# Kernel tuning notes

Measured on AMD Instinct MI355X. Metric: run time of the kernel, lower is better.

The kernel has to match this reference:

```python
import jax, jax.numpy as jnp
import numpy as np
from jax.scipy.linalg import solve_triangular

LS = 0.5414            # frozen GP length scale (_gp_scale.data = 0.5414)
L2 = LS * LS
D = 2
K_OPS = D + 2          # operators: identity, d/dx_i (i=1..d), laplacian
JITTER_KXX = 1e-5
JITTER_AKA = 1e-4
JITTER_YY = 1e-5


def _opiK(xout, xin, l2, d):
    # op_i applied to first arg of RBF kernel -> (bs, k, m, n)
    r = xout[:, :, None, :] - xin[:, None, :, :]            # (bs,m,n,d)
    u = jnp.sum(r * r, axis=-1) / l2                        # (bs,m,n)
    K = jnp.exp(-0.5 * u)
    ri = jnp.moveaxis(r, -1, 1)                             # (bs,d,m,n)
    grad = -(ri / l2) * K[:, None]                          # d/dx_i K
    lap = ((u - d) / l2) * K                                # Lap_x K
    return jnp.concatenate([K[:, None], grad, lap[:, None]], axis=1)


def _opiKopjfull(x, l2, d):
    # op_i on first arg, op_j on second arg -> (bs, k, k, m, m)
    r = x[:, :, None, :] - x[:, None, :, :]
    u = jnp.sum(r * r, axis=-1) / l2
    K = jnp.exp(-0.5 * u)
    ri = jnp.moveaxis(r, -1, 1)                             # (bs,d,m,m)
    gK = (ri / l2) * K[:, None]                             # d/dy_j K
    lapK = ((u - d) / l2) * K                               # Lap K (either arg)
    eye = jnp.eye(d, dtype=x.dtype)[None, :, :, None, None]
    gg = (eye / l2 - ri[:, :, None] * ri[:, None] / (l2 * l2)) * K[:, None, None]  # d/dx_i d/dy_j K
    glap = (ri / (l2 * l2)) * (((2.0 + d - u) * K)[:, None])  # d/dx_i Lap_y K
    laplap = (((u - d) ** 2 - 4.0 * u + 2.0 * d) / (l2 * l2)) * K  # Lap_x Lap_y K
    row0 = jnp.concatenate([K[:, None, None], gK[:, None], lapK[:, None, None]], axis=2)
    rowg = jnp.concatenate([(-gK)[:, :, None], gg, glap[:, :, None]], axis=2)
    rowl = jnp.concatenate([lapK[:, None, None], (-glap)[:, None], laplap[:, None, None]], axis=2)
    return jnp.concatenate([row0, rowg, rowl], axis=1)


def _psd_solve(L, B):
    # (Kxx + jitter I)^{-1} B via Cholesky (stands in for gpytorch inv_matmul/CG)
    y = solve_triangular(L, B, lower=True)
    return solve_triangular(L, y, lower=True, trans=1)


def _forward(xin, meanin, Kin, weight, bias):
    bs, n, c = meanin.shape
    d, k, l2 = D, K_OPS, L2
    xout, m = xin, n
    r = xin[:, :, None, :] - xin[:, None, :, :]
    Kxx = jnp.exp(-0.5 * jnp.sum(r * r, axis=-1) / l2)      # (bs,n,n)
    In = jnp.eye(n, dtype=xin.dtype)
    Lc = jnp.linalg.cholesky(Kxx + JITTER_KXX * In)
    opiKmn = _opiK(xout, xin, l2, d)                        # (bs,k,m,n)
    # posterior mean of op_i applied to the GP
    opimean = (opiKmn.reshape(bs, k * m, n) @ _psd_solve(Lc, meanin)).reshape(bs, k, m, c)
    Amean = jnp.transpose(opimean, (0, 2, 3, 1)).reshape(bs, m, c * k) @ weight.T + bias
    W = weight.reshape(-1, c, k)                            # (cout,c,k)
    W2 = jnp.einsum('oci,ocj->ij', W, W) / W.shape[0]       # (k,k)
    Kxxinvopi = jnp.swapaxes(
        _psd_solve(Lc, jnp.swapaxes(opiKmn.reshape(bs, k * m, n), 1, 2)), 1, 2)  # (bs,km,n)
    interp_weights = jnp.swapaxes(_psd_solve(Lc, Kin), 1, 2)                      # (bs,n,n)
    opi_interp = jnp.transpose((Kxxinvopi @ interp_weights).reshape(bs, k, m, n), (0, 2, 3, 1))  # (bs,m,n,k)
    Ak_interp = (opi_interp @ W2).reshape(bs, m, n * k)
    Im = jnp.eye(m, dtype=xin.dtype)
    AkinA = Ak_interp @ jnp.transpose(opiKmn, (0, 3, 1, 2)).reshape(bs, n * k, m) + JITTER_AKA * Im
    opiKxxxopj = jnp.transpose(
        (Kxxinvopi @ jnp.swapaxes(opiKmn.reshape(bs, k * m, n), 1, 2)).reshape(bs, k, m, k, m),
        (0, 1, 3, 2, 4))                                    # (bs,k,k,m,m)
    ijkyy = _opiKopjfull(xout, l2, d) - opiKxxxopj          # posterior cov of op_i f, op_j f
    AkAyy = jnp.einsum('bijmp,ij->bmp', ijkyy, W2) + JITTER_YY * Im
    full_AKA = AkinA + AkAyy
    return (xout, Amean, full_AKA)


def setup_inputs() -> dict:
    bs, n, cin, cout = 4, 576, 32, 64
    key = jax.random.key(0)
    k1, k2, k3, k4, k5 = jax.random.split(key, 5)
    xin = jax.random.uniform(k1, (bs, n, D), dtype=jnp.float32) * 6.0
    meanin = jax.random.normal(k2, (bs, n, cin), dtype=jnp.float32)
    A = jax.random.normal(k3, (bs, n, n), dtype=jnp.float32) / np.float32(np.sqrt(n))
    Kin = A @ jnp.swapaxes(A, 1, 2) + 0.1 * jnp.eye(n, dtype=jnp.float32)  # PSD covariance
    fan_in = cin * K_OPS
    weight = jax.random.normal(k4, (cout, fan_in), dtype=jnp.float32) / np.float32(np.sqrt(fan_in))
    bias = jax.random.normal(k5, (cout,), dtype=jnp.float32) * 0.01
    return {"xin": xin, "meanin": meanin, "Kin": Kin, "weight": weight, "bias": bias}


def reference(xin, meanin, Kin, weight, bias):
    return _forward(xin, meanin, Kin, weight, bias)
```

## Files before the change

### kernel.cpp

```cpp
#include <hip/hip_runtime.h>
#include <math.h>

#define NPTS 576
#define N2 331776
#define BSZ 4
#define NB 64
#define NT 9

#define INVL2 (1.0f/0.29311396f)

typedef __attribute__((ext_vector_type(8))) short short8v;
typedef __attribute__((ext_vector_type(16))) float f32x16;

__global__ void build_k(const float* __restrict__ xin,
                        float* __restrict__ Kxx, float* __restrict__ opiK,
                        float* __restrict__ out) {
    int idx = blockIdx.x * 256 + threadIdx.x;
    if (idx < 4608) out[idx] = xin[idx];
    int b = idx / N2;
    int rem = idx - b * N2;
    int m = rem / NPTS;
    int nn = rem - m * NPTS;
    const float* xb = xin + (size_t)b * NPTS * 2;
    float xm0 = xb[m*2],  xm1 = xb[m*2+1];
    float xn0 = xb[nn*2], xn1 = xb[nn*2+1];
    float r0 = xm0 - xn0, r1 = xm1 - xn1;
    float u = (r0*r0 + r1*r1) * INVL2;
    float Kv = expf(-0.5f * u);
    Kxx[idx] = Kv + ((m == nn) ? 1e-5f : 0.0f);
    size_t base = (size_t)b * 4 * N2 + rem;
    opiK[base]          = Kv;
    opiK[base + N2]     = -r0 * INVL2 * Kv;
    opiK[base + 2*N2]   = -r1 * INVL2 * Kv;
    opiK[base + 3*N2]   = (u - 2.0f) * INVL2 * Kv;
}

__global__ void w2_k(const float* __restrict__ w, float* __restrict__ W2) {
    __shared__ float red[256];
    int tid = threadIdx.x;
    int pair = tid & 15;
    int slice = tid >> 4;
    int i = pair >> 2, j = pair & 3;
    float s = 0.0f;
    for (int o = slice * 4; o < slice * 4 + 4; ++o)
        for (int c = 0; c < 32; ++c)
            s += w[o*128 + c*4 + i] * w[o*128 + c*4 + j];
    red[tid] = s;
    __syncthreads();
    if (tid < 16) {
        float t = 0.0f;
        #pragma unroll
        for (int k = 0; k < 16; ++k) t += red[pair + 16*k];
        W2[pair] = t * (1.0f/64.0f);
    }
}

__device__ void factor_invert_64(float (*T)[NB+1], float (*V)[NB+1],
                                 float (*tmp)[17], int tid) {
    for (int p = 0; p < 4; ++p) {
        int cp = p * 16;
        if (tid < 64) {
            int r = tid;
            float reg[16];
            #pragma unroll
            for (int q = 0; q < 16; ++q) reg[q] = T[r][cp + q];
            #pragma unroll
            for (int j = 0; j < 16; ++j) {
                int col = cp + j;
                float d2 = __shfl(reg[j], col);
                float d = sqrtf(fmaxf(d2, 1e-12f));
                float lr = (r == col) ? d : reg[j] / d;
                reg[j] = lr;
                #pragma unroll
                for (int q = j + 1; q < 16; ++q) {
                    float lc = __shfl(lr, cp + q);
                    if (r >= cp + q) reg[q] -= lr * lc;
                }
            }
            #pragma unroll
            for (int q = 0; q < 16; ++q) T[r][cp + q] = reg[q];
        }
        __syncthreads();
        int tr = 48 - cp;
        if (tr > 0) {
            for (int idx = tid; idx < tr * tr; idx += 256) {
                int r = cp + 16 + idx / tr;
                int c = cp + 16 + idx % tr;
                if (c <= r) {
                    float s = 0.0f;
                    #pragma unroll
                    for (int k = 0; k < 16; ++k) s += T[r][cp+k] * T[c][cp+k];
                    T[r][c] -= s;
                }
            }
        }
        __syncthreads();
    }
    if (tid < 64) {
        int I = tid >> 4, c = tid & 15, base = I * 16;
        float tcol[16];
        #pragma unroll
        for (int i = 0; i < 16; ++i) tcol[i] = T[base + i][base + c];
        float v[16];
        #pragma unroll
        for (int i = 0; i < 16; ++i) {
            float s = (i == c) ? 1.0f : 0.0f;
            #pragma unroll
            for (int k = 0; k < 16; ++k) {
                if (k < i) {
                    float tik = __shfl(tcol[i], base + k);
                    s -= tik * v[k];
                }
            }
            float tii = __shfl(tcol[i], base + i);
            v[i] = s / tii;
        }
        #pragma unroll
        for (int i = 0; i < 16; ++i) V[base + i][base + c] = v[i];
    }
    __syncthreads();
    const int PI[6] = {1,2,3,2,3,3};
    const int PJ[6] = {0,1,2,0,1,0};
    int rr16 = tid >> 4, cc16 = tid & 15;
    for (int p = 0; p < 6; ++p) {
        int I = PI[p], J = PJ[p];
        float s = 0.0f;
        for (int K = J; K < I; ++K)
            #pragma unroll
            for (int t = 0; t < 16; ++t)
                s += T[I*16+rr16][K*16+t] * V[K*16+t][J*16+cc16];
        tmp[rr16][cc16] = s;
        __syncthreads();
        float s2 = 0.0f;
        for (int t = 0; t <= rr16; ++t) s2 += V[I*16+rr16][I*16+t] * tmp[t][cc16];
        __syncthreads();
        V[I*16+rr16][J*16+cc16] = -s2;
        __syncthreads();
    }
}

__global__ void chol_diag0(const float* __restrict__ A, float* __restrict__ LinvKK,
                           float* __restrict__ VTKK) {
    int b = blockIdx.x;
    const float* Ab = A + (size_t)b * N2;
    __shared__ float T[NB][NB+1];
    __shared__ float V[NB][NB+1];
    __shared__ float tmp[16][17];
    int tid = threadIdx.x;
    for (int idx = tid; idx < NB*NB; idx += 256) {
        int r = idx >> 6, c = idx & 63;
        T[r][c] = Ab[(size_t)r * NPTS + c];
        V[r][c] = 0.0f;
    }
    __syncthreads();
    factor_invert_64(T, V, tmp, tid);
    float* Vg  = LinvKK + (size_t)b * NT * NB * NB;
    float* VTg = VTKK  + (size_t)b * NT * NB * NB;
    for (int idx = tid; idx < NB*NB; idx += 256) {
        Vg[idx]  = V[idx >> 6][idx & 63];
        VTg[idx] = V[idx & 63][idx >> 6];
    }
}

__global__ __launch_bounds__(256)
void chol_step(float* __restrict__ A, float* __restrict__ LT,
               float* __restrict__ LinvKK, float* __restrict__ VTKK, int kb) {
    int b = blockIdx.y;
    int p = blockIdx.x;
    int ir = 0;
    while (p >= ir + 1) { p -= ir + 1; ir++; }
    int ib = kb + 1 + ir, jb = kb + 1 + p;
    float* Ab = A + (size_t)b * N2;
    float* LTb = LT + (size_t)b * N2;
    __shared__ float Ai[NB][NB+1];
    __shared__ float Aj[NB][NB+1];
    __shared__ float Vs[NB][NB+1];
    __shared__ float tmp[16][17];
    int tid = threadIdx.x;
    int tx = tid & 15, ty = tid >> 4;
    const float* Vg = LinvKK + ((size_t)b * NT + kb) * NB * NB;
    bool diag = (ib == jb);
    for (int idx = tid; idx < NB*NB; idx += 256) {
        int r = idx >> 6, c = idx & 63;
        Ai[r][c] = Ab[(size_t)(ib*NB + r) * NPTS + kb*NB + c];
        Aj[r][c] = diag ? 0.0f : Ab[(size_t)(jb*NB + r) * NPTS + kb*NB + c];
        Vs[r][c] = Vg[idx];
    }
    float U[4][4];
    #pragma unroll
    for (int i = 0; i < 4; ++i)
        #pragma unroll
        for (int j = 0; j < 4; ++j)
            U[i][j] = Ab[(size_t)(ib*NB + ty*4+i) * NPTS + jb*NB + tx*4+j];
    __syncthreads();
    float Li[4][4] = {}, Lj[4][4] = {};
    for (int k = 0; k < NB; ++k) {
        float a[4], v[4];
        #pragma unroll
        for (int i = 0; i < 4; ++i) a[i] = Ai[ty*4+i][k];
        #pragma unroll
        for (int j = 0; j < 4; ++j) v[j] = Vs[tx*4+j][k];
        #pragma unroll
        for (int i = 0; i < 4; ++i)
            #pragma unroll
            for (int j = 0; j < 4; ++j) Li[i][j] += a[i] * v[j];
        if (!diag) {
            float aj[4];
            #pragma unroll
            for (int i = 0; i < 4; ++i) aj[i] = Aj[ty*4+i][k];
            #pragma unroll
            for (int i = 0; i < 4; ++i)
                #pragma unroll
                for (int j = 0; j < 4; ++j) Lj[i][j] += aj[i] * v[j];
        }
    }
    __syncthreads();
    #pragma unroll
    for (int i = 0; i < 4; ++i)
        #pragma unroll
        for (int j = 0; j < 4; ++j) {
            Ai[ty*4+i][tx*4+j] = Li[i][j];
            Aj[ty*4+i][tx*4+j] = diag ? Li[i][j] : Lj[i][j];
        }
    if (diag) {
        #pragma unroll
        for (int i = 0; i < 4; ++i)
            #pragma unroll
            for (int j = 0; j < 4; ++j)
                LTb[(size_t)(kb*NB + tx*4+j) * NPTS + ib*NB + ty*4+i] = Li[i][j];
    }
    __syncthreads();
    float s[4][4] = {};
    for (int k = 0; k < NB; ++k) {
        float a[4], v[4];
        #pragma unroll
        for (int i = 0; i < 4; ++i) a[i] = Ai[ty*4+i][k];
        #pragma unroll
        for (int j = 0; j < 4; ++j) v[j] = Aj[tx*4+j][k];
        #pragma unroll
        for (int i = 0; i < 4; ++i)
            #pragma unroll
            for (int j = 0; j < 4; ++j) s[i][j] += a[i] * v[j];
    }
    #pragma unroll
    for (int i = 0; i < 4; ++i)
        #pragma unroll
        for (int j = 0; j < 4; ++j) U[i][j] -= s[i][j];
    if (blockIdx.x != 0) {
        #pragma unroll
        for (int i = 0; i < 4; ++i)
            #pragma unroll
            for (int j = 0; j < 4; ++j)
                Ab[(size_t)(ib*NB + ty*4+i) * NPTS + jb*NB + tx*4+j] = U[i][j];
        return;
    }
    __syncthreads();
    #pragma unroll
    for (int i = 0; i < 4; ++i)
        #pragma unroll
        for (int j = 0; j < 4; ++j) Ai[ty*4+i][tx*4+j] = U[i][j];
    for (int idx = tid; idx < NB*NB; idx += 256) Aj[idx >> 6][idx & 63] = 0.0f;
    __syncthreads();
    factor_invert_64(Ai, Aj, tmp, tid);
    float* Vo  = LinvKK + ((size_t)b * NT + (kb + 1)) * NB * NB;
    float* VTo = VTKK  + ((size_t)b * NT + (kb + 1)) * NB * NB;
    for (int idx = tid; idx < NB*NB; idx += 256) {
        Vo[idx]  = Aj[idx >> 6][idx & 63];
        VTo[idx] = Aj[idx & 63][idx >> 6];
    }
}

__global__ __launch_bounds__(256)
void trinv_blk(const float* __restrict__ LT, const float* __restrict__ LinvKK,
               const float* __restrict__ VTKK, float* __restrict__ Linv) {
    int sp = blockIdx.x, jb = blockIdx.y, b = blockIdx.z;
    const float* LTb = LT + (size_t)b * N2;
    float* Xg = Linv + (size_t)b * N2;
    const float* Vg  = LinvKK + (size_t)b * NT * NB * NB;
    const float* VTg = VTKK  + (size_t)b * NT * NB * NB;
    int c0 = jb * NB + sp * 16;

    __shared__ float LsT[64][72];
    __shared__ float Xc[576][17];
    __shared__ float Ss[64][17];

    int tid = threadIdx.x;
    int tx = tid & 15, ty = tid >> 4;
    int st = tid >> 2, sc = (tid & 3) * 16;

    {
        const float* Vjj = Vg + (size_t)jb * NB * NB;
        int r = tid >> 2, c4 = (tid & 3) * 4;
        float4 v = *(const float4*)(Vjj + r * NB + sp * 16 + c4);
        Xc[r][c4+0] = v.x; Xc[r][c4+1] = v.y; Xc[r][c4+2] = v.z; Xc[r][c4+3] = v.w;
        *(float4*)(Xg + (size_t)(jb * NB + r) * NPTS + c0 + c4) = v;
    }
    __syncthreads();

    for (int ib = jb + 1; ib < NT; ++ib) {
        float acc[4] = {};
        for (int kb = jb; kb < ib; ++kb) {
            {
                const float* src = LTb + (size_t)(kb * NB + st) * NPTS + ib * NB + sc;
                #pragma unroll
                for (int q = 0; q < 4; ++q)
                    *(float4*)&LsT[st][sc + q*4] = *(const float4*)(src + q*4);
            }
            __syncthreads();
            int xbase = (kb - jb) * 64;
            #pragma unroll 8
            for (int t = 0; t < 64; ++t) {
                float a4[4]; *(float4*)a4 = *(const float4*)&LsT[t][ty*4];
                float xv = Xc[xbase + t][tx];
                #pragma unroll
                for (int i = 0; i < 4; ++i) acc[i] += a4[i] * xv;
            }
            __syncthreads();
        }
        #pragma unroll
        for (int i = 0; i < 4; ++i) Ss[ty*4+i][tx] = acc[i];
        {
            const float* VTi = VTg + (size_t)ib * NB * NB;
            const float* src = VTi + st * NB + sc;
            #pragma unroll
            for (int q = 0; q < 4; ++q)
                *(float4*)&LsT[st][sc + q*4] = *(const float4*)(src + q*4);
        }
        __syncthreads();
        float acc2[4] = {};
        #pragma unroll 8
        for (int t = 0; t < 64; ++t) {
            float a4[4]; *(float4*)a4 = *(const float4*)&LsT[t][ty*4];
            float sv = Ss[t][tx];
            #pragma unroll
            for (int i = 0; i < 4; ++i) acc2[i] += a4[i] * sv;
        }
        int obase = (ib - jb) * 64;
        #pragma unroll
        for (int i = 0; i < 4; ++i) {
            float v = -acc2[i];
            Xc[obase + ty*4 + i][tx] = v;
            Xg[(size_t)(ib * NB + ty*4 + i) * NPTS + c0 + tx] = v;
        }
        __syncthreads();
    }
}

__device__ inline void split3(float v, unsigned short& h0, unsigned short& h1,
                              unsigned short& h2) {
    unsigned u0 = __float_as_uint(v) & 0xffff0000u;
    float f0 = __uint_as_float(u0);
    float r1 = v - f0;
    unsigned u1 = __float_as_uint(r1) & 0xffff0000u;
    float f1 = __uint_as_float(u1);
    float r2 = r1 - f1;
    h0 = (unsigned short)(u0 >> 16);
    h1 = (unsigned short)(u1 >> 16);
    h2 = (unsigned short)((__float_as_uint(r2) + 0x8000u) >> 16);
}

__device__ inline void pack_store(unsigned short* dst, const unsigned short* v) {
    uint4 w;
    w.x = (unsigned)v[0] | ((unsigned)v[1] << 16);
    w.y = (unsigned)v[2] | ((unsigned)v[3] << 16);
    w.z = (unsigned)v[4] | ((unsigned)v[5] << 16);
    w.w = (unsigned)v[6] | ((unsigned)v[7] << 16);
    *(uint4*)dst = w;
}

template<int EPIB>
__global__ __launch_bounds__(256, 2)
void mm_p2_mfma(const float* __restrict__ Aall, const float* __restrict__ Ball,
                float* __restrict__ Call, long sA, long sB, long sC)
{
    int id = blockIdx.x;
    int x8 = id & 7, qq = id >> 3;
    int nx = qq % 9;
    int band = x8 + 8 * (qq / 9);
    if (band >= 18 * BSZ) return;
    int t  = band % 18;
    int b  = band / 18;
    int pp = t / 9, my = t % 9;
    const float* A0 = Aall + (size_t)b * sA + (size_t)(pp * 2) * N2;
    const float* A1 = A0 + N2;
    const float* B  = Ball + (size_t)b * sB;
    float* C0 = Call + (size_t)b * sC + (size_t)(pp * 2) * N2;
    float* C1 = C0 + N2;
    int n0 = nx * 64, m0 = my * 64;

    __shared__ __align__(16) unsigned short As[12][2][64][8];
    __shared__ __align__(16) unsigned short Bs[6][2][64][8];

    int tid  = threadIdx.x;
    int lane = tid & 63;
    int wid  = tid >> 6;
    int wr = wid >> 1, wc = wid & 1;

    f32x16 acc0, acc1;
    #pragma unroll
    for (int i = 0; i < 16; ++i) { acc0[i] = 0.0f; acc1[i] = 0.0f; }

    int ap   = tid >> 7;
    int aq   = tid & 127;
    int ar   = aq >> 1;
    int asub = aq & 1;
    const float* Apl = ap ? A1 : A0;
    int areg = ar >> 5;
    int aln  = ar & 31;

    int bc   = tid & 63;
    int bkg  = tid >> 6;
    int bsub = bkg >> 1;
    int bln  = (bc & 31) + 32 * (bkg & 1);
    int bwc  = bc >> 5;

    float av[16];
    float bv[8];

    auto loadA = [&](int k0) {
        const float* p = Apl + (size_t)(m0 + ar) * 576 + k0 + asub * 16;
        float4 t0 = *(const float4*)(p);
        float4 t1 = *(const float4*)(p + 4);
        float4 t2 = *(const float4*)(p + 8);
        float4 t3 = *(const float4*)(p + 12);
        av[0]=t0.x;  av[1]=t0.y;  av[2]=t0.z;  av[3]=t0.w;
        av[4]=t1.x;  av[5]=t1.y;  av[6]=t1.z;  av[7]=t1.w;
        av[8]=t2.x;  av[9]=t2.y;  av[10]=t2.z; av[11]=t2.w;
        av[12]=t3.x; av[13]=t3.y; av[14]=t3.z; av[15]=t3.w;
    };
    auto loadB = [&](int k0) {
        const float* p = B + (size_t)(k0 + bkg * 8) * 576 + n0 + bc;
        #pragma unroll
        for (int j = 0; j < 8; ++j) {
            float v = p[(size_t)j * 576];
            if (EPIB) { if (k0 + bkg * 8 + j == n0 + bc) v -= 1.0f; }
            bv[j] = v;
        }
    };
    auto storeA = [&]() {
        unsigned short s0[16], s1[16], s2[16];
        #pragma unroll
        for (int j = 0; j < 16; ++j) split3(av[j], s0[j], s1[j], s2[j]);
        #pragma unroll
        for (int h = 0; h < 2; ++h) {
            int ln = aln + 32 * h;
            pack_store(&As[(ap*3 + 0)*2 + areg][asub][ln][0], &s0[8*h]);
            pack_store(&As[(ap*3 + 1)*2 + areg][asub][ln][0], &s1[8*h]);
            pack_store(&As[(ap*3 + 2)*2 + areg][asub][ln][0], &s2[8*h]);
        }
    };
    auto storeB = [&]() {
        unsigned short s0[8], s1[8], s2[8];
        #pragma unroll
        for (int j = 0; j < 8; ++j) split3(bv[j], s0[j], s1[j], s2[j]);
        pack_store(&Bs[0*2 + bwc][bsub][bln][0], s0);
        pack_store(&Bs[1*2 + bwc][bsub][bln][0], s1);
        pack_store(&Bs[2*2 + bwc][bsub][bln][0], s2);
    };

    const short8v* Af = (const short8v*)As;
    const short8v* Bf = (const short8v*)Bs;

    loadA(0); loadB(0);
    for (int k0 = 0; k0 < 576; k0 += 32) {
        storeA(); storeB();
        __syncthreads();
        if (k0 + 32 < 576) { loadA(k0 + 32); loadB(k0 + 32); }
        #pragma unroll
        for (int sub = 0; sub < 2; ++sub) {
            short8v b0 = Bf[((0*2 + wc)*2 + sub)*64 + lane];
            short8v b1 = Bf[((1*2 + wc)*2 + sub)*64 + lane];
            short8v b2 = Bf[((2*2 + wc)*2 + sub)*64 + lane];
            short8v a0 = Af[((0*3 + 0)*2 + wr)*128 + sub*64 + lane];
            short8v a1 = Af[((0*3 + 1)*2 + wr)*128 + sub*64 + lane];
            short8v a2 = Af[((0*3 + 2)*2 + wr)*128 + sub*64 + lane];
            acc0 = __builtin_amdgcn_mfma_f32_32x32x16_bf16(a0, b0, acc0, 0, 0, 0);
            acc0 = __builtin_amdgcn_mfma_f32_32x32x16_bf16(a0, b1, acc0, 0, 0, 0);
            acc0 = __builtin_amdgcn_mfma_f32_32x32x16_bf16(a1, b0, acc0, 0, 0, 0);
            acc0 = __builtin_amdgcn_mfma_f32_32x32x16_bf16(a1, b1, acc0, 0, 0, 0);
            acc0 = __builtin_amdgcn_mfma_f32_32x32x16_bf16(a0, b2, acc0, 0, 0, 0);
            acc0 = __builtin_amdgcn_mfma_f32_32x32x16_bf16(a2, b0, acc0, 0, 0, 0);
            a0 = Af[((1*3 + 0)*2 + wr)*128 + sub*64 + lane];
            a1 = Af[((1*3 + 1)*2 + wr)*128 + sub*64 + lane];
            a2 = Af[((1*3 + 2)*2 + wr)*128 + sub*64 + lane];
            acc1 = __builtin_amdgcn_mfma_f32_32x32x16_bf16(a0, b0, acc1, 0, 0, 0);
            acc1 = __builtin_amdgcn_mfma_f32_32x32x16_bf16(a0, b1, acc1, 0, 0, 0);
            acc1 = __builtin_amdgcn_mfma_f32_32x32x16_bf16(a1, b0, acc1, 0, 0, 0);
            acc1 = __builtin_amdgcn_mfma_f32_32x32x16_bf16(a1, b1, acc1, 0, 0, 0);
            acc1 = __builtin_amdgcn_mfma_f32_32x32x16_bf16(a0, b2, acc1, 0, 0, 0);
            acc1 = __builtin_amdgcn_mfma_f32_32x32x16_bf16(a2, b0, acc1, 0, 0, 0);
        }
        __syncthreads();
    }

    int colg = n0 + 32*wc + (lane & 31);
    int rowb = m0 + 32*wr + 4*(lane >> 5);
    #pragma unroll
    for (int reg = 0; reg < 16; ++reg) {
        int row = rowb + (reg & 3) + 8*(reg >> 2);
        C0[(size_t)row * 576 + colg] = acc0[reg];
        C1[(size_t)row * 576 + colg] = acc1[reg];
    }
}

__global__ __launch_bounds__(256, 2)
void mm_abt_mfma(const float* __restrict__ Aall, const float* __restrict__ Ball,
                 float* __restrict__ Call, long sA, long sB, long sC, long sSplit)
{
    int p = blockIdx.x;
    int ir = 0;
    while (p >= ir + 1) { p -= ir + 1; ir++; }
    int my = ir, nx = p;
    int zz = blockIdx.z;
    int sp = zz & 3, b = zz >> 2;
    const float* A = Aall + (size_t)b * sA + (size_t)sp * N2;
    const float* B = Ball + (size_t)b * sB + (size_t)sp * N2;
    float* Cp = Call + (size_t)b * sC + (size_t)sp * sSplit;
    int m0 = my * 64, n0 = nx * 64;

    __shared__ __align__(16) unsigned short Fr[12][2][64][8];

    int tid  = threadIdx.x;
    int lane = tid & 63;
    int wid  = tid >> 6;
    int wr = wid >> 1, wc = wid & 1;

    f32x16 acc;
    #pragma unroll
    for (int i = 0; i < 16; ++i) acc[i] = 0.0f;

    int sel  = tid >> 7;
    int q2   = tid & 127;
    int r    = q2 >> 1;
    int ssub = q2 & 1;
    const float* Src = sel ? B : A;
    int base0 = sel ? n0 : m0;
    int rreg = r >> 5;
    int rln  = r & 31;

    float av[16];

    auto loadF = [&](int k0) {
        const float* pp = Src + (size_t)(base0 + r) * 576 + k0 + ssub * 16;
        float4 t0 = *(const float4*)(pp);
        float4 t1 = *(const float4*)(pp + 4);
        float4 t2 = *(const float4*)(pp + 8);
        float4 t3 = *(const float4*)(pp + 12);
        av[0]=t0.x;  av[1]=t0.y;  av[2]=t0.z;  av[3]=t0.w;
        av[4]=t1.x;  av[5]=t1.y;  av[6]=t1.z;  av[7]=t1.w;
        av[8]=t2.x;  av[9]=t2.y;  av[10]=t2.z; av[11]=t2.w;
        av[12]=t3.x; av[13]=t3.y; av[14]=t3.z; av[15]=t3.w;
    };
    auto storeF = [&]() {
        unsigned short s0[16], s1[16], s2[16];
        #pragma unroll
        for (int j = 0; j < 16; ++j) split3(av[j], s0[j], s1[j], s2[j]);
        #pragma unroll
        for (int h = 0; h < 2; ++h) {
            int ln = rln + 32 * h;
            pack_store(&Fr[sel*6 + 0*2 + rreg][ssub][ln][0], &s0[8*h]);
            pack_store(&Fr[sel*6 + 1*2 + rreg][ssub][ln][0], &s1[8*h]);
            pack_store(&Fr[sel*6 + 2*2 + rreg][ssub][ln][0], &s2[8*h]);
        }
    };

    const short8v* Ff = (const short8v*)Fr;

    loadF(0);
    for (int k0 = 0; k0 < 576; k0 += 32) {
        storeF();
        __syncthreads();
        if (k0 + 32 < 576) loadF(k0 + 32);
        #pragma unroll
        for (int sub = 0; sub < 2; ++sub) {
            short8v a0 = Ff[((0*2 + wr)*2 + sub)*64 + lane];
            short8v a1 = Ff[((1*2 + wr)*2 + sub)*64 + lane];
            short8v a2 = Ff[((2*2 + wr)*2 + sub)*64 + lane];
            short8v b0 = Ff[((6 + 0*2 + wc)*2 + sub)*64 + lane];
            short8v b1 = Ff[((6 + 1*2 + wc)*2 + sub)*64 + lane];
            short8v b2 = Ff[((6 + 2*2 + wc)*2 + sub)*64 + lane];
            acc = __builtin_amdgcn_mfma_f32_32x32x16_bf16(a0, b0, acc, 0, 0, 0);
            acc = __builtin_amdgcn_mfma_f32_32x32x16_bf16(a0, b1, acc, 0, 0, 0);
            acc = __builtin_amdgcn_mfma_f32_32x32x16_bf16(a1, b0, acc, 0, 0, 0);
            acc = __builtin_amdgcn_mfma_f32_32x32x16_bf16(a1, b1, acc, 0, 0, 0);
            acc = __builtin_amdgcn_mfma_f32_32x32x16_bf16(a0, b2, acc, 0, 0, 0);
            acc = __builtin_amdgcn_mfma_f32_32x32x16_bf16(a2, b0, acc, 0, 0, 0);
        }
        __syncthreads();
    }

    int colg = n0 + 32*wc + (lane & 31);
    int rowb = m0 + 32*wr + 4*(lane >> 5);
    #pragma unroll
    for (int reg = 0; reg < 16; ++reg) {
        int row = rowb + (reg & 3) + 8*(reg >> 2);
        Cp[(size_t)row * 576 + colg] = acc[reg];
    }
}

__global__ __launch_bounds__(256, 2)
void mm_ata_mfma(const float* __restrict__ Lg, float* __restrict__ C,
                 long sA, long sC)
{
    int p = blockIdx.x;
    int ir = 0;
    while (p >= ir + 1) { p -= ir + 1; ir++; }
    int my = ir, nx = p;
    int b = blockIdx.z;
    const float* A = Lg + (size_t)b * sA;
    float* Cb = C + (size_t)b * sC;
    int m0 = my * 64, n0 = nx * 64;
    int kBeg = m0;

    __shared__ __align__(16) unsigned short Fr[12][2][64][8];

    int tid  = threadIdx.x;
    int lane = tid & 63;
    int wid  = tid >> 6;
    int wr = wid >> 1, wc = wid & 1;

    f32x16 acc;
    #pragma unroll
    for (int i = 0; i < 16; ++i) acc[i] = 0.0f;

    int sel  = tid >> 7;
    int q2   = tid & 127;
    int col  = q2 & 63;
    int ssub = q2 >> 6;
    int c0base = sel ? n0 : m0;
    int rreg = col >> 5;
    int rln  = col & 31;

    float av[16];

    auto loadF = [&](int k0) {
        const float* pp = A + (size_t)(k0 + ssub * 16) * 576 + c0base + col;
        #pragma unroll
        for (int j = 0; j < 16; ++j) av[j] = pp[(size_t)j * 576];
    };
    auto storeF = [&]() {
        unsigned short s0[16], s1[16], s2[16];
        #pragma unroll
        for (int j = 0; j < 16; ++j) split3(av[j], s0[j], s1[j], s2[j]);
        #pragma unroll
        for (int h = 0; h < 2; ++h) {
            int ln = rln + 32 * h;
            pack_store(&Fr[sel*6 + 0*2 + rreg][ssub][ln][0], &s0[8*h]);
            pack_store(&Fr[sel*6 + 1*2 + rreg][ssub][ln][0], &s1[8*h]);
            pack_store(&Fr[sel*6 + 2*2 + rreg][ssub][ln][0], &s2[8*h]);
        }
    };

    const short8v* Ff = (const short8v*)Fr;

    loadF(kBeg);
    for (int k0 = kBeg; k0 < 576; k0 += 32) {
        storeF();
        __syncthreads();
        if (k0 + 32 < 576) loadF(k0 + 32);
        #pragma unroll
        for (int sub = 0; sub < 2; ++sub) {
            short8v a0 = Ff[((0*2 + wr)*2 + sub)*64 + lane];
            short8v a1 = Ff[((1*2 + wr)*2 + sub)*64 + lane];
            short8v a2 = Ff[((2*2 + wr)*2 + sub)*64 + lane];
            short8v b0 = Ff[((6 + 0*2 + wc)*2 + sub)*64 + lane];
            short8v b1 = Ff[((6 + 1*2 + wc)*2 + sub)*64 + lane];
            short8v b2 = Ff[((6 + 2*2 + wc)*2 + sub)*64 + lane];
            acc = __builtin_amdgcn_mfma_f32_32x32x16_bf16(a0, b0, acc, 0, 0, 0);
            acc = __builtin_amdgcn_mfma_f32_32x32x16_bf16(a0, b1, acc, 0, 0, 0);
            acc = __builtin_amdgcn_mfma_f32_32x32x16_bf16(a1, b0, acc, 0, 0, 0);
            acc = __builtin_amdgcn_mfma_f32_32x32x16_bf16(a1, b1, acc, 0, 0, 0);
            acc = __builtin_amdgcn_mfma_f32_32x32x16_bf16(a0, b2, acc, 0, 0, 0);
            acc = __builtin_amdgcn_mfma_f32_32x32x16_bf16(a2, b0, acc, 0, 0, 0);
        }
        __syncthreads();
    }

    int colg = n0 + 32*wc + (lane & 31);
    int rowb = m0 + 32*wr + 4*(lane >> 5);
    #pragma unroll
    for (int reg = 0; reg < 16; ++reg) {
        int row = rowb + (reg & 3) + 8*(reg >> 2);
        float v = acc[reg];
        Cb[(size_t)row * 576 + colg] = v;
        Cb[(size_t)colg * 576 + row] = v;
    }
}

__global__ __launch_bounds__(256, 2)
void mm_ab_mfma(const float* __restrict__ Aall, const float* __restrict__ Ball,
                float* __restrict__ Call, long sA, long sB, long sC)
{
    int nx = blockIdx.x % 9, my = blockIdx.x / 9;
    int b = blockIdx.z;
    const float* A = Aall + (size_t)b * sA;
    const float* B = Ball + (size_t)b * sB;
    float* Cb = Call + (size_t)b * sC;
    int m0 = my * 64, n0 = nx * 64;

    __shared__ __align__(16) unsigned short Fr[12][2][64][8];

    int tid  = threadIdx.x;
    int lane = tid & 63;
    int wid  = tid >> 6;
    int wr = wid >> 1, wc = wid & 1;

    f32x16 acc;
    #pragma unroll
    for (int i = 0; i < 16; ++i) acc[i] = 0.0f;

    int sel  = tid >> 7;
    int q2   = tid & 127;
    int ar   = q2 >> 1;
    int asub = q2 & 1;
    int areg = ar >> 5, aln = ar & 31;
    int bcol = q2 & 63;
    int bssub = q2 >> 6;
    int breg = bcol >> 5, brln = bcol & 31;

    float av[16];

    auto loadF = [&](int k0) {
        if (sel == 0) {
            const float* pp = A + (size_t)(m0 + ar) * 576 + k0 + asub * 16;
            float4 t0 = *(const float4*)(pp);
            float4 t1 = *(const float4*)(pp + 4);
            float4 t2 = *(const float4*)(pp + 8);
            float4 t3 = *(const float4*)(pp + 12);
            av[0]=t0.x;  av[1]=t0.y;  av[2]=t0.z;  av[3]=t0.w;
            av[4]=t1.x;  av[5]=t1.y;  av[6]=t1.z;  av[7]=t1.w;
            av[8]=t2.x;  av[9]=t2.y;  av[10]=t2.z; av[11]=t2.w;
            av[12]=t3.x; av[13]=t3.y; av[14]=t3.z; av[15]=t3.w;
        } else {
            const float* pp = B + (size_t)(k0 + bssub * 16) * 576 + n0 + bcol;
            #pragma unroll
            for (int j = 0; j < 16; ++j) av[j] = pp[(size_t)j * 576];
        }
    };
    auto storeF = [&]() {
        unsigned short s0[16], s1[16], s2[16];
        #pragma unroll
        for (int j = 0; j < 16; ++j) split3(av[j], s0[j], s1[j], s2[j]);
        int reg0 = sel ? (6 + 0*2 + breg) : (0*2 + areg);
        int reg1 = sel ? (6 + 1*2 + breg) : (1*2 + areg);
        int reg2 = sel ? (6 + 2*2 + breg) : (2*2 + areg);
        int sb   = sel ? bssub : asub;
        int ln0  = sel ? brln : aln;
        #pragma unroll
        for (int h = 0; h < 2; ++h) {
            int ln = ln0 + 32 * h;
            pack_store(&Fr[reg0][sb][ln][0], &s0[8*h]);
            pack_store(&Fr[reg1][sb][ln][0], &s1[8*h]);
            pack_store(&Fr[reg2][sb][ln][0], &s2[8*h]);
        }
    };

    const short8v* Ff = (const short8v*)Fr;

    loadF(0);
    for (int k0 = 0; k0 < 576; k0 += 32) {
        storeF();
        __syncthreads();
        if (k0 + 32 < 576) loadF(k0 + 32);
        #pragma unroll
        for (int sub = 0; sub < 2; ++sub) {
            short8v a0 = Ff[((0*2 + wr)*2 + sub)*64 + lane];
            short8v a1 = Ff[((1*2 + wr)*2 + sub)*64 + lane];
            short8v a2 = Ff[((2*2 + wr)*2 + sub)*64 + lane];
            short8v b0 = Ff[((6 + 0*2 + wc)*2 + sub)*64 + lane];
            short8v b1 = Ff[((6 + 1*2 + wc)*2 + sub)*64 + lane];
            short8v b2 = Ff[((6 + 2*2 + wc)*2 + sub)*64 + lane];
            acc = __builtin_amdgcn_mfma_f32_32x32x16_bf16(a0, b0, acc, 0, 0, 0);
            acc = __builtin_amdgcn_mfma_f32_32x32x16_bf16(a0, b1, acc, 0, 0, 0);
            acc = __builtin_amdgcn_mfma_f32_32x32x16_bf16(a1, b0, acc, 0, 0, 0);
            acc = __builtin_amdgcn_mfma_f32_32x32x16_bf16(a1, b1, acc, 0, 0, 0);
            acc = __builtin_amdgcn_mfma_f32_32x32x16_bf16(a0, b2, acc, 0, 0, 0);
            acc = __builtin_amdgcn_mfma_f32_32x32x16_bf16(a2, b0, acc, 0, 0, 0);
        }
        __syncthreads();
    }

    int colg = n0 + 32*wc + (lane & 31);
    int rowb = m0 + 32*wr + 4*(lane >> 5);
    #pragma unroll
    for (int reg = 0; reg < 16; ++reg) {
        int row = rowb + (reg & 3) + 8*(reg >> 2);
        Cb[(size_t)row * 576 + colg] = acc[reg];
    }
}

template<int TA, int TB, int SK, int TRI, int SWZ, int EPIB, int TRIC>
__global__ __launch_bounds__(256)
void mm_kernel(const float* __restrict__ Aall, const float* __restrict__ Ball,
               float* __restrict__ Call,
               int M, int N, int K, int planeK,
               int lda, int ldb, int ldc,
               long sA, long sB, long sC, long pA, long pB, long sSplit, int MT)
{
    int nx, my, zz;
    if (TRIC) {
        int p = blockIdx.x;
        int ir = 0;
        while (p >= ir + 1) { p -= ir + 1; ir++; }
        my = ir; nx = p; zz = blockIdx.z;
    } else if (SWZ) {
        int id = blockIdx.x;
        int x8 = id & 7;
        int q  = id >> 3;
        nx = q % 9;
        int band = x8 + 8 * (q / 9);
        if (band >= MT * 4 * SK) return;
        my = band % MT;
        zz = band / MT;
    } else { nx = blockIdx.x; my = blockIdx.y; zz = blockIdx.z; }
    int sp = (SK > 1) ? (zz % SK) : 0;
    int b  = (SK > 1) ? (zz / SK) : zz;
    const float* A = Aall + (size_t)b * sA;
    const float* B = Ball + (size_t)b * sB;
    float* C = Call + (size_t)b * sC + (size_t)sp * sSplit;
    int n0 = nx * 64;
    int m0 = my * 64;

    __shared__ float As[16][68];
    __shared__ float Bs[16][68];

    int tid = threadIdx.x;
    int tx = tid & 15, ty = tid >> 4;

    float acc[4][4] = {};
    bool mFull = (m0 + 64 <= M);
    bool nFull = (n0 + 64 <= N);

    int triBeg = 0;
    if (TRI) { int mx = (m0 > n0 ? m0 : n0); triBeg = mx & ~15; }
    int kBeg = triBeg, kEnd = K;
    if (SK > 1) {
        int len = K - triBeg;
        int chunk = ((len / SK) + 15) & ~15;
        kBeg = triBeg + sp * chunk;
        if (kBeg > K) kBeg = K;
        kEnd = (sp == SK - 1) ? K : (kBeg + chunk < K ? kBeg + chunk : K);
    }

    float avr[4];
    float bvr[4];

    auto loadA = [&](int k0) {
        int plane = k0 / planeK;
        int koff  = k0 - plane * planeK;
        if (TA == 0) {
            const float* Ab = A + (size_t)pA * plane;
            int r = tid >> 2, c4 = (tid & 3) * 4;
            int gm = m0 + r;
            if (mFull || gm < M) {
                float4 t = *(const float4*)(Ab + (size_t)gm * lda + koff + c4);
                avr[0]=t.x; avr[1]=t.y; avr[2]=t.z; avr[3]=t.w;
            } else { avr[0]=avr[1]=avr[2]=avr[3]=0.0f; }
        } else {
            int r = tid >> 4, c4 = (tid & 15) * 4;
            const float* p = A + (size_t)(koff + r) * lda + m0 + c4;
            if (mFull) {
                float4 t = *(const float4*)p;
                avr[0]=t.x; avr[1]=t.y; avr[2]=t.z; avr[3]=t.w;
            } else {
                #pragma unroll
                for (int jj = 0; jj < 4; ++jj)
                    avr[jj] = (m0 + c4 + jj < M) ? p[jj] : 0.0f;
            }
        }
    };
    auto storeA = [&]() {
        if (TA == 0) {
            int r = tid >> 2, c4 = (tid & 3) * 4;
            #pragma unroll
            for (int q = 0; q < 4; ++q) As[c4+q][r] = avr[q];
        } else {
            int r = tid >> 4, c4 = (tid & 15) * 4;
            #pragma unroll
            for (int q = 0; q < 4; ++q) As[r][c4+q] = avr[q];
        }
    };
    auto loadB = [&](int k0) {
        int plane = k0 / planeK;
        int koff  = k0 - plane * planeK;
        if (TB == 0) {
            int r = tid >> 4, c4 = (tid & 15) * 4;
            const float* p = B + (size_t)(koff + r) * ldb + n0 + c4;
            if (nFull) {
                float4 t = *(const float4*)p;
                bvr[0]=t.x; bvr[1]=t.y; bvr[2]=t.z; bvr[3]=t.w;
            } else {
                #pragma unroll
                for (int jj = 0; jj < 4; ++jj)
                    bvr[jj] = (n0 + c4 + jj < N) ? p[jj] : 0.0f;
            }
            if (EPIB) {
                int gk = koff + r;
                #pragma unroll
                for (int jj = 0; jj < 4; ++jj)
                    if (gk == n0 + c4 + jj) bvr[jj] -= 1.0f;
            }
        } else {
            const float* Bb = B + (size_t)pB * plane;
            int r = tid >> 2, c4 = (tid & 3) * 4;
            int gp = n0 + r;
            if (nFull || gp < N) {
                float4 t = *(const float4*)(Bb + (size_t)gp * ldb + koff + c4);
                bvr[0]=t.x; bvr[1]=t.y; bvr[2]=t.z; bvr[3]=t.w;
            } else { bvr[0]=bvr[1]=bvr[2]=bvr[3]=0.0f; }
        }
    };
    auto storeB = [&]() {
        if (TB == 0) {
            int r = tid >> 4, c4 = (tid & 15) * 4;
            #pragma unroll
            for (int q = 0; q < 4; ++q) Bs[r][c4+q] = bvr[q];
        } else {
            int r = tid >> 2, c4 = (tid & 3) * 4;
            #pragma unroll
            for (int q = 0; q < 4; ++q) Bs[c4+q][r] = bvr[q];
        }
    };

    if (kBeg < kEnd) {
        loadA(kBeg); loadB(kBeg);
        for (int k0 = kBeg; k0 < kEnd; k0 += 16) {
            storeA(); storeB();
            __syncthreads();
            if (k0 + 16 < kEnd) { loadA(k0 + 16); loadB(k0 + 16); }
            #pragma unroll
            for (int kk = 0; kk < 16; ++kk) {
                float a[4], bb[4];
                *(float4*)a  = *(const float4*)&As[kk][ty*4];
                *(float4*)bb = *(const float4*)&Bs[kk][tx*4];
                #pragma unroll
                for (int i = 0; i < 4; ++i)
                    #pragma unroll
                    for (int j = 0; j < 4; ++j)
                        acc[i][j] += a[i] * bb[j];
            }
            __syncthreads();
        }
    }

    #pragma unroll
    for (int i = 0; i < 4; ++i) {
        int gm = m0 + ty*4 + i;
        if (gm >= M) continue;
        #pragma unroll
        for (int j = 0; j < 4; ++j) {
            int gn = n0 + tx*4 + j;
            if (gn >= N) continue;
            C[(size_t)gm * ldc + gn] = acc[i][j];
        }
    }
}

__global__ void combine_solm4(const float* __restrict__ p, float* __restrict__ o) {
    int i = blockIdx.x * 256 + threadIdx.x;
    o[i] = p[i] + p[i + 73728] + p[i + 2*73728] + p[i + 3*73728];
}

__global__ void combine_prior4_sym(const float* __restrict__ p0,
                                   const float* __restrict__ xin,
                                   const float* __restrict__ W2g,
                                   float* __restrict__ o, long stride) {
    __shared__ float w[16];
    int tid = threadIdx.x;
    if (tid < 16) w[tid] = W2g[tid];
    __syncthreads();
    int idx = blockIdx.x * 256 + tid;
    int b = idx / N2;
    int rem = idx - b * N2;
    int m = rem / NPTS, n = rem - m * NPTS;
    if (m < n) return;
    const float* xb = xin + (size_t)b * NPTS * 2;
    float r0 = xb[m*2+0] - xb[n*2+0];
    float r1 = xb[m*2+1] - xb[n*2+1];
    float u = (r0*r0 + r1*r1) * INVL2;
    float Kv = expf(-0.5f * u);
    float i2 = INVL2 * INVL2;
    float gK0 = r0 * INVL2 * Kv;
    float gK1 = r1 * INVL2 * Kv;
    float lapK = (u - 2.0f) * INVL2 * Kv;
    float gg00 = (INVL2 - r0*r0*i2) * Kv;
    float gg01 = (-r0*r1*i2) * Kv;
    float gg11 = (INVL2 - r1*r1*i2) * Kv;
    float gl0 = r0 * i2 * (4.0f - u) * Kv;
    float gl1 = r1 * i2 * (4.0f - u) * Kv;
    float ll = ((u-2.0f)*(u-2.0f) - 4.0f*u + 4.0f) * i2 * Kv;
    float prior =
          w[0]*Kv + w[1]*gK0 + w[2]*gK1 + w[3]*lapK
        + w[4]*(-gK0) + w[5]*gg00 + w[6]*gg01 + w[7]*gl0
        + w[8]*(-gK1) + w[9]*gg01 + w[10]*gg11 + w[11]*gl1
        + w[12]*lapK + w[13]*(-gl0) + w[14]*(-gl1) + w[15]*ll;
    float v = p0[idx] + p0[idx + stride] + p0[idx + 2*stride] + p0[idx + 3*stride]
            + prior;
    if (m == n) v += 1.1e-4f;
    o[(size_t)b * N2 + (size_t)m * NPTS + n] = v;
    if (m != n)
        o[(size_t)b * N2 + (size_t)n * NPTS + m] = v;
}

__global__ void opiw2_k(const float* __restrict__ opiK, const float* __restrict__ W2,
                        float* __restrict__ outB) {
    int idx = blockIdx.x * 256 + threadIdx.x;
    int b = idx / N2;
    int rem = idx - b * N2;
    size_t base = (size_t)b * 4 * N2 + rem;
    float k0 = opiK[base], k1 = opiK[base + N2], k2 = opiK[base + 2*N2], k3 = opiK[base + 3*N2];
    #pragma unroll
    for (int i = 0; i < 4; ++i)
        outB[base + (size_t)i * N2] = W2[i*4+0]*k0 + W2[i*4+1]*k1 + W2[i*4+2]*k2 + W2[i*4+3]*k3;
}

__global__ __launch_bounds__(256)
void amean_k(const float* __restrict__ opimean, const float* __restrict__ weight,
             const float* __restrict__ bias, float* __restrict__ out) {
    int b = blockIdx.y;
    int m0 = blockIdx.x * 32;
    __shared__ float Wl[64][128];
    __shared__ float om[32][128];
    int tid = threadIdx.x;
    for (int idx = tid; idx < 64*128; idx += 256) Wl[idx / 128][idx & 127] = weight[idx];
    for (int idx = tid; idx < 32*128; idx += 256) {
        int m = idx >> 7, ck = idx & 127, c = ck >> 2, kop = ck & 3;
        om[m][ck] = opimean[((size_t)b * 4 + kop) * NPTS * 32 + (size_t)(m0 + m) * 32 + c];
    }
    __syncthreads();
    int ml = tid >> 3, o0 = (tid & 7) * 8;
    float acc[8] = {};
    for (int ck = 0; ck < 128; ++ck) {
        float v = om[ml][ck];
        #pragma unroll
        for (int q = 0; q < 8; ++q) acc[q] += v * Wl[o0+q][ck];
    }
    #pragma unroll
    for (int q = 0; q < 8; ++q)
        out[4608 + ((size_t)b * NPTS + m0 + ml) * 64 + o0 + q] = acc[q] + bias[o0+q];
}

static inline int gridSwz(int MT, int Z) { return 8 * 9 * ((MT * Z + 7) / 8); }

extern "C" void kernel_launch(void* const* d_in, const int* in_sizes, int n_in,
                              void* d_out, int out_size, void* d_ws, size_t ws_size,
                              hipStream_t stream) {
    const float* xin    = (const float*)d_in[0];
    const float* meanin = (const float*)d_in[1];
    const float* Kin    = (const float*)d_in[2];
    const float* weight = (const float*)d_in[3];
    const float* bias   = (const float*)d_in[4];
    float* out = (float*)d_out;
    float* ws  = (float*)d_ws;

    const long N2L = N2;
    float* W2      = ws;
    float* LinvKK  = ws + 64;
    float* VTKK    = LinvKK + 147456;
    float* R1 = VTKK + 147456;
    float* R2 = R1 + 4*N2L;
    float* R3 = R2 + 4*N2L;
    float* R4 = R3 + 4*N2L;
    float* R5 = R4 + 16*N2L;
    float* R6 = R5 + 16*N2L;

    hipMemsetAsync(R2, 0, (size_t)4 * N2 * sizeof(float), stream);
    build_k<<<dim3((BSZ*N2)/256), dim3(256), 0, stream>>>(xin, R1, R4, out);
    w2_k<<<dim3(1), dim3(256), 0, stream>>>(weight, W2);
    chol_diag0<<<dim3(BSZ), dim3(256), 0, stream>>>(R1, LinvKK, VTKK);
    for (int kb = 0; kb < NT - 1; ++kb) {
        int t = NT - 1 - kb;
        chol_step<<<dim3(t*(t+1)/2, BSZ), dim3(256), 0, stream>>>(
            R1, R5, LinvKK, VTKK, kb);
    }
    trinv_blk<<<dim3(4, NT, BSZ), dim3(256), 0, stream>>>(R5, LinvKK, VTKK, R2);
    mm_ata_mfma<<<dim3(45, 1, BSZ), dim3(256), 0, stream>>>(R2, R3, N2L, N2L);
    mm_kernel<0,0,4,0,0,0,0><<<dim3(1,9,16), dim3(256), 0, stream>>>(
        R3, meanin, R6, 576,32,576,576, 576,32,32,
        N2L,18432,18432, 0,0, 73728, 9);
    combine_solm4<<<dim3(288), dim3(256), 0, stream>>>(R6, R2);
    mm_kernel<0,0,1,0,0,0,0><<<dim3(1,36,BSZ), dim3(256), 0, stream>>>(
        R4, R2, R2 + 73728, 2304,32,576,576, 576,32,32,
        4*N2L,18432,73728, 0,0, 0, 9);
    amean_k<<<dim3(18,BSZ), dim3(256), 0, stream>>>(R2 + 73728, weight, bias, out);
    mm_ab_mfma<<<dim3(81, 1, BSZ), dim3(256), 0, stream>>>(
        Kin, R3, R1, N2L, N2L, N2L);
    mm_p2_mfma<0><<<dim3(gridSwz(18,4)), dim3(256), 0, stream>>>(
        R4, R3, R5, 4*N2L, N2L, 4*N2L);
    opiw2_k<<<dim3((BSZ*N2)/256), dim3(256), 0, stream>>>(R4, W2, R4);
    mm_p2_mfma<1><<<dim3(gridSwz(18,4)), dim3(256), 0, stream>>>(
        R5, R1, R6, 4*N2L, N2L, 4*N2L);
    mm_abt_mfma<<<dim3(45,1,BSZ*4), dim3(256), 0, stream>>>(
        R6, R4, R5, 4*N2L, 4*N2L, N2L, 4*N2L);
    combine_prior4_sym<<<dim3(5184), dim3(256), 0, stream>>>(
        R5, xin, W2, out + 152064, 4*N2L);
}
```

Before: 895.1 us.

## Fuse small launches, drop memset, prefetch tiles in triangular inverse

Computes the W2 weight Gram matrix inside the last block of build_k instead of a separate launch. The memset of the inverse buffer is replaced by trinv_blk zeroing its own upper-triangle region. The split-K solve-mean matmul plus its combine kernel become a single non-split matmul. trinv_blk also register-prefetches the next L/V tile during compute. The aim is to cut launch count and hide global load latency, at the cost of less parallelism in the solve-mean matmul.

```diff
diff --git a/kernel.cpp b/kernel.cpp
--- a/kernel.cpp
+++ b/kernel.cpp
@@ -14,7 +14,8 @@
 
 __global__ void build_k(const float* __restrict__ xin,
                         float* __restrict__ Kxx, float* __restrict__ opiK,
-                        float* __restrict__ out) {
+                        float* __restrict__ out,
+                        const float* __restrict__ w, float* __restrict__ W2) {
     int idx = blockIdx.x * 256 + threadIdx.x;
     if (idx < 4608) out[idx] = xin[idx];
     int b = idx / N2;
@@ -33,25 +34,24 @@
     opiK[base + N2]     = -r0 * INVL2 * Kv;
     opiK[base + 2*N2]   = -r1 * INVL2 * Kv;
     opiK[base + 3*N2]   = (u - 2.0f) * INVL2 * Kv;
-}
-
-__global__ void w2_k(const float* __restrict__ w, float* __restrict__ W2) {
-    __shared__ float red[256];
-    int tid = threadIdx.x;
-    int pair = tid & 15;
-    int slice = tid >> 4;
-    int i = pair >> 2, j = pair & 3;
-    float s = 0.0f;
-    for (int o = slice * 4; o < slice * 4 + 4; ++o)
-        for (int c = 0; c < 32; ++c)
-            s += w[o*128 + c*4 + i] * w[o*128 + c*4 + j];
-    red[tid] = s;
-    __syncthreads();
-    if (tid < 16) {
-        float t = 0.0f;
-        #pragma unroll
-        for (int k = 0; k < 16; ++k) t += red[pair + 16*k];
-        W2[pair] = t * (1.0f/64.0f);
+    if (blockIdx.x == 5183) {
+        __shared__ float red[256];
+        int tid = threadIdx.x;
+        int pair = tid & 15;
+        int slice = tid >> 4;
+        int i = pair >> 2, j = pair & 3;
+        float s = 0.0f;
+        for (int o = slice * 4; o < slice * 4 + 4; ++o)
+            for (int c = 0; c < 32; ++c)
+                s += w[o*128 + c*4 + i] * w[o*128 + c*4 + j];
+        red[tid] = s;
+        __syncthreads();
+        if (tid < 16) {
+            float t = 0.0f;
+            #pragma unroll
+            for (int k = 0; k < 16; ++k) t += red[pair + 16*k];
+            W2[pair] = t * (1.0f/64.0f);
+        }
     }
 }
 
@@ -289,24 +289,46 @@
     int st = tid >> 2, sc = (tid & 3) * 16;
 
     {
+        float4 z = {0.0f, 0.0f, 0.0f, 0.0f};
+        for (int i = tid; i < jb * NB * 4; i += 256) {
+            int r = i >> 2, q = i & 3;
+            *(float4*)(Xg + (size_t)r * NPTS + c0 + q * 4) = z;
+        }
+    }
+
+    float4 pf[4];
+    auto issueL = [&](int ib, int kb) {
+        const float* src = LTb + (size_t)(kb * NB + st) * NPTS + ib * NB + sc;
+        #pragma unroll
+        for (int q = 0; q < 4; ++q) pf[q] = *(const float4*)(src + q * 4);
+    };
+    auto issueV = [&](int ib) {
+        const float* src = VTg + (size_t)ib * NB * NB + st * NB + sc;
+        #pragma unroll
+        for (int q = 0; q < 4; ++q) pf[q] = *(const float4*)(src + q * 4);
+    };
+    auto commit = [&]() {
+        #pragma unroll
+        for (int q = 0; q < 4; ++q) *(float4*)&LsT[st][sc + q * 4] = pf[q];
+    };
+
+    {
         const float* Vjj = Vg + (size_t)jb * NB * NB;
         int r = tid >> 2, c4 = (tid & 3) * 4;
         float4 v = *(const float4*)(Vjj + r * NB + sp * 16 + c4);
         Xc[r][c4+0] = v.x; Xc[r][c4+1] = v.y; Xc[r][c4+2] = v.z; Xc[r][c4+3] = v.w;
         *(float4*)(Xg + (size_t)(jb * NB + r) * NPTS + c0 + c4) = v;
     }
+    if (jb + 1 < NT) issueL(jb + 1, jb);
     __syncthreads();
 
     for (int ib = jb + 1; ib < NT; ++ib) {
         float acc[4] = {};
         for (int kb = jb; kb < ib; ++kb) {
-            {
-                const float* src = LTb + (size_t)(kb * NB + st) * NPTS + ib * NB + sc;
-                #pragma unroll
-                for (int q = 0; q < 4; ++q)
-                    *(float4*)&LsT[st][sc + q*4] = *(const float4*)(src + q*4);
-            }
+            commit();
             __syncthreads();
+            if (kb + 1 < ib) issueL(ib, kb + 1);
+            else             issueV(ib);
             int xbase = (kb - jb) * 64;
             #pragma unroll 8
             for (int t = 0; t < 64; ++t) {
@@ -317,16 +339,11 @@
             }
             __syncthreads();
         }
+        commit();
         #pragma unroll
         for (int i = 0; i < 4; ++i) Ss[ty*4+i][tx] = acc[i];
-        {
-            const float* VTi = VTg + (size_t)ib * NB * NB;
-            const float* src = VTi + st * NB + sc;
-            #pragma unroll
-            for (int q = 0; q < 4; ++q)
-                *(float4*)&LsT[st][sc + q*4] = *(const float4*)(src + q*4);
-        }
-        __syncthreads();
+        __syncthreads();
+        if (ib + 1 < NT) issueL(ib + 1, jb);
         float acc2[4] = {};
         #pragma unroll 8
         for (int t = 0; t < 64; ++t) {
@@ -954,11 +971,6 @@
             C[(size_t)gm * ldc + gn] = acc[i][j];
         }
     }
-}
-
-__global__ void combine_solm4(const float* __restrict__ p, float* __restrict__ o) {
-    int i = blockIdx.x * 256 + threadIdx.x;
-    o[i] = p[i] + p[i + 73728] + p[i + 2*73728] + p[i + 3*73728];
 }
 
 __global__ void combine_prior4_sym(const float* __restrict__ p0,
@@ -1064,9 +1076,8 @@
     float* R5 = R4 + 16*N2L;
     float* R6 = R5 + 16*N2L;
 
-    hipMemsetAsync(R2, 0, (size_t)4 * N2 * sizeof(float), stream);
-    build_k<<<dim3((BSZ*N2)/256), dim3(256), 0, stream>>>(xin, R1, R4, out);
-    w2_k<<<dim3(1), dim3(256), 0, stream>>>(weight, W2);
+    build_k<<<dim3((BSZ*N2)/256), dim3(256), 0, stream>>>(
+        xin, R1, R4, out, weight, W2);
     chol_diag0<<<dim3(BSZ), dim3(256), 0, stream>>>(R1, LinvKK, VTKK);
     for (int kb = 0; kb < NT - 1; ++kb) {
         int t = NT - 1 - kb;
@@ -1075,10 +1086,9 @@
     }
     trinv_blk<<<dim3(4, NT, BSZ), dim3(256), 0, stream>>>(R5, LinvKK, VTKK, R2);
     mm_ata_mfma<<<dim3(45, 1, BSZ), dim3(256), 0, stream>>>(R2, R3, N2L, N2L);
-    mm_kernel<0,0,4,0,0,0,0><<<dim3(1,9,16), dim3(256), 0, stream>>>(
-        R3, meanin, R6, 576,32,576,576, 576,32,32,
-        N2L,18432,18432, 0,0, 73728, 9);
-    combine_solm4<<<dim3(288), dim3(256), 0, stream>>>(R6, R2);
+    mm_kernel<0,0,1,0,0,0,0><<<dim3(1,9,BSZ), dim3(256), 0, stream>>>(
+        R3, meanin, R2, 576,32,576,576, 576,32,32,
+        N2L,18432,18432, 0,0, 0, 9);
     mm_kernel<0,0,1,0,0,0,0><<<dim3(1,36,BSZ), dim3(256), 0, stream>>>(
         R4, R2, R2 + 73728, 2304,32,576,576, 576,32,32,
         4*N2L,18432,73728, 0,0, 0, 9);
```

After: 914.2 us. 2.1% more time.
